# Performance work log

Hardware: AMD Instinct MI355X
Metric: run time of the kernel (lower is better)

Reference implementation:

```python
import jax, jax.numpy as jnp
import numpy as np

B, LQ, LKV, D = 32, 1024, 1024, 512

def setup_inputs() -> dict:
    key = jax.random.key(0)
    kq, kkv = jax.random.split(key)
    query = jax.random.normal(kq, (B, LQ, D), dtype=jnp.float32)
    key_value = jax.random.normal(kkv, (B, LKV, D), dtype=jnp.float32)
    return {"query": query, "key_value": key_value}

def reference(query, key_value):
    # scores: [B, Lq, Lkv] (unscaled dot-product attention)
    scores = jnp.einsum('bqd,bkd->bqk', query, key_value)
    attn_score = jax.nn.softmax(scores, axis=-1)
    # output: [B, Lq, D]
    output = jnp.einsum('bqk,bkd->bqd', attn_score, key_value)
    return (output, attn_score)
```

## Files before the change

### kernel.cpp

```cpp
#include <hip/hip_runtime.h>


constexpr int NB  = 32;
constexpr int LQ  = 1024;
constexpr int LKV = 1024;
constexpr int DD  = 512;

typedef __attribute__((ext_vector_type(4))) float f4;
typedef __attribute__((ext_vector_type(4))) float f32x4;
typedef __attribute__((ext_vector_type(4))) unsigned short u16x4;
typedef __attribute__((ext_vector_type(8))) __bf16 bf16x8;

__device__ __forceinline__ unsigned short f2bf(float x) {
  unsigned u = __builtin_bit_cast(unsigned, x);
  unsigned r = u + 0x7FFFu + ((u >> 16) & 1u);
  return (unsigned short)(r >> 16);
}
__device__ __forceinline__ float bf2f(unsigned short h) {
  unsigned u = ((unsigned)h) << 16;
  return __builtin_bit_cast(float, u);
}

__device__ __forceinline__ void gload16(const void* g, void* l) {
  __builtin_amdgcn_global_load_lds((const __attribute__((address_space(1))) unsigned int*)g,
                                   (__attribute__((address_space(3))) unsigned int*)l,
                                   16, 0, 0);
}

constexpr int PAD = 40;

__global__ __launch_bounds__(256) void gemm_qk_kernel(const float* __restrict__ Q,
                                                      const float* __restrict__ KV,
                                                      float* __restrict__ S)
{
  __shared__ unsigned short Ah[128][PAD], Al[128][PAD], Bh[128][PAD], Bl[128][PAD];
  const int b   = blockIdx.y;
  const int ti  = blockIdx.x >> 3;
  const int tj  = blockIdx.x & 7;
  const int tid  = threadIdx.x;
  const int lane = tid & 63;
  const int wid  = tid >> 6;
  const int wr = (wid >> 1) * 64;
  const int wc = (wid & 1) * 64;

  const float* Qb = Q  + (size_t)b * LQ  * DD + (size_t)ti * 128 * DD;
  const float* Kb = KV + (size_t)b * LKV * DD + (size_t)tj * 128 * DD;

  f32x4 acc[4][4] = {};

  for (int ks = 0; ks < DD; ks += 32) {
    __syncthreads();
#pragma unroll
    for (int i = 0; i < 4; ++i) {
      int idx = tid + i * 256;
      int r   = idx >> 3;
      int k4  = (idx & 7) << 2;
      f4 qa = *(const f4*)(Qb + (size_t)r * DD + ks + k4);
      f4 ka = *(const f4*)(Kb + (size_t)r * DD + ks + k4);
      u16x4 qh, ql, kh, kl;
#pragma unroll
      for (int u = 0; u < 4; ++u) {
        unsigned short h = f2bf(qa[u]);
        qh[u] = h;  ql[u] = f2bf(qa[u] - bf2f(h));
        unsigned short h2 = f2bf(ka[u]);
        kh[u] = h2; kl[u] = f2bf(ka[u] - bf2f(h2));
      }
      *(u16x4*)&Ah[r][k4] = qh;  *(u16x4*)&Al[r][k4] = ql;
      *(u16x4*)&Bh[r][k4] = kh;  *(u16x4*)&Bl[r][k4] = kl;
    }
    __syncthreads();

    const int kf = (lane >> 4) << 3;
    bf16x8 ah[4], al[4], bh[4], bl[4];
#pragma unroll
    for (int m = 0; m < 4; ++m) {
      int row = wr + m * 16 + (lane & 15);
      ah[m] = *(const bf16x8*)&Ah[row][kf];
      al[m] = *(const bf16x8*)&Al[row][kf];
    }
#pragma unroll
    for (int n = 0; n < 4; ++n) {
      int row = wc + n * 16 + (lane & 15);
      bh[n] = *(const bf16x8*)&Bh[row][kf];
      bl[n] = *(const bf16x8*)&Bl[row][kf];
    }
#pragma unroll
    for (int m = 0; m < 4; ++m)
#pragma unroll
      for (int n = 0; n < 4; ++n) {
        acc[m][n] = __builtin_amdgcn_mfma_f32_16x16x32_bf16(ah[m], bh[n], acc[m][n], 0, 0, 0);
        acc[m][n] = __builtin_amdgcn_mfma_f32_16x16x32_bf16(ah[m], bl[n], acc[m][n], 0, 0, 0);
        acc[m][n] = __builtin_amdgcn_mfma_f32_16x16x32_bf16(al[m], bh[n], acc[m][n], 0, 0, 0);
      }
  }

  float* Sb = S + (size_t)b * LQ * LKV;
#pragma unroll
  for (int m = 0; m < 4; ++m) {
    int row0 = ti * 128 + wr + m * 16 + ((lane >> 4) << 2);
#pragma unroll
    for (int n = 0; n < 4; ++n) {
      int col = tj * 128 + wc + n * 16 + (lane & 15);
#pragma unroll
      for (int j = 0; j < 4; ++j)
        Sb[(size_t)(row0 + j) * LKV + col] = acc[m][n][j];
    }
  }
}

__global__ __launch_bounds__(256) void softmax_kernel(float* __restrict__ S)
{
  __shared__ float redmax[4], redsum[4];
  const int tid = threadIdx.x;
  float* p = S + (size_t)blockIdx.x * LKV;

  f4 v = *(const f4*)(p + tid * 4);
  float mx = fmaxf(fmaxf(v[0], v[1]), fmaxf(v[2], v[3]));
#pragma unroll
  for (int off = 32; off >= 1; off >>= 1)
    mx = fmaxf(mx, __shfl_xor(mx, off));
  if ((tid & 63) == 0) redmax[tid >> 6] = mx;
  __syncthreads();
  mx = fmaxf(fmaxf(redmax[0], redmax[1]), fmaxf(redmax[2], redmax[3]));

  f4 e;
#pragma unroll
  for (int u = 0; u < 4; ++u) e[u] = __expf(v[u] - mx);
  float sm = e[0] + e[1] + e[2] + e[3];
#pragma unroll
  for (int off = 32; off >= 1; off >>= 1)
    sm += __shfl_xor(sm, off);
  if ((tid & 63) == 0) redsum[tid >> 6] = sm;
  __syncthreads();
  sm = redsum[0] + redsum[1] + redsum[2] + redsum[3];

  float inv = 1.0f / sm;
  f4 o = { e[0] * inv, e[1] * inv, e[2] * inv, e[3] * inv };
  *(f4*)(p + tid * 4) = o;
}

__global__ __launch_bounds__(256) void kvt_prep_kernel(const float* __restrict__ KV,
                                                       unsigned short* __restrict__ KVT)
{
  __shared__ unsigned short T[64][72];
  const int b  = blockIdx.z;
  const int tk = blockIdx.y;
  const int td = blockIdx.x;
  const int tid = threadIdx.x;

#pragma unroll
  for (int i = 0; i < 4; ++i) {
    int idx = tid + i * 256;
    int r   = idx >> 4;
    int c4  = (idx & 15) << 2;
    f4 v = *(const f4*)(KV + ((size_t)b * LKV + tk * 64 + r) * DD + td * 64 + c4);
    u16x4 h;
#pragma unroll
    for (int u = 0; u < 4; ++u) h[u] = f2bf(v[u]);
    *(u16x4*)&T[r][c4] = h;
  }
  __syncthreads();

#pragma unroll
  for (int i = 0; i < 4; ++i) {
    int idx = tid + i * 256;
    int c   = idx >> 4;
    int r4  = (idx & 15) << 2;
    u16x4 w = { T[r4][c], T[r4 + 1][c], T[r4 + 2][c], T[r4 + 3][c] };
    *(u16x4*)(KVT + ((size_t)b * DD + td * 64 + c) * LKV + tk * 64 + r4) = w;
  }
}

__global__ __launch_bounds__(512) void gemm_av2_kernel(const float* __restrict__ A,
                                                       const unsigned short* __restrict__ KVT,
                                                       float* __restrict__ O)
{
  __shared__ unsigned short Asm[128][72];
  __shared__ unsigned short Bsm[256 * 64];
  const int b  = blockIdx.z;
  const int mi = blockIdx.y;
  const int nj = blockIdx.x;
  const int tid  = threadIdx.x;
  const int lane = tid & 63;
  const int wid  = tid >> 6;
  const int wr = (wid >> 2) * 64;
  const int wc = (wid & 3) * 64;

  const float* Ab = A + (size_t)b * LQ * LKV + (size_t)mi * 128 * LKV;
  const unsigned short* Bb = KVT + ((size_t)b * DD + nj * 256) * LKV;

  f32x4 acc[4][4] = {};

  for (int ks = 0; ks < LKV; ks += 64) {
    __syncthreads();
#pragma unroll
    for (int i = 0; i < 4; ++i) {
      int idx = tid + i * 512;
      int r   = idx >> 4;
      int k4  = (idx & 15) << 2;
      f4 v = *(const f4*)(Ab + (size_t)r * LKV + ks + k4);
      u16x4 h;
#pragma unroll
      for (int u = 0; u < 4; ++u) h[u] = f2bf(v[u]);
      *(u16x4*)&Asm[r][k4] = h;
    }
#pragma unroll
    for (int c = 0; c < 4; ++c) {
      int cc = wid * 4 + c;
      int dd = cc * 8 + (lane >> 3);
      int ss = (lane & 7) ^ (dd & 7);
      const unsigned short* g = Bb + (size_t)dd * LKV + ks + ss * 8;
      gload16(g, &Bsm[cc * 512]);
    }
    __syncthreads();

#pragma unroll
    for (int kk = 0; kk < 64; kk += 32) {
      const int kf = kk + ((lane >> 4) << 3);
      const int cl = kf >> 3;
      bf16x8 af[4], bfv[4];
#pragma unroll
      for (int m = 0; m < 4; ++m)
        af[m] = *(const bf16x8*)&Asm[wr + m * 16 + (lane & 15)][kf];
#pragma unroll
      for (int n = 0; n < 4; ++n) {
        int dd = wc + n * 16 + (lane & 15);
        int sp = cl ^ (dd & 7);
        bfv[n] = *(const bf16x8*)&Bsm[dd * 64 + sp * 8];
      }
#pragma unroll
      for (int m = 0; m < 4; ++m)
#pragma unroll
        for (int n = 0; n < 4; ++n)
          acc[m][n] = __builtin_amdgcn_mfma_f32_16x16x32_bf16(af[m], bfv[n], acc[m][n], 0, 0, 0);
    }
  }

  float* Ob = O + (size_t)b * LQ * DD;
#pragma unroll
  for (int m = 0; m < 4; ++m) {
    int row0 = mi * 128 + wr + m * 16 + ((lane >> 4) << 2);
#pragma unroll
    for (int n = 0; n < 4; ++n) {
      int col = nj * 256 + wc + n * 16 + (lane & 15);
#pragma unroll
      for (int j = 0; j < 4; ++j)
        Ob[(size_t)(row0 + j) * DD + col] = acc[m][n][j];
    }
  }
}

__global__ __launch_bounds__(256) void gemm_av_kernel(const float* __restrict__ A,
                                                      const float* __restrict__ KV,
                                                      float* __restrict__ O)
{
  __shared__ unsigned short Ab[128][PAD], Bt[128][PAD];
  const int b  = blockIdx.z;
  const int mi = blockIdx.y;
  const int nj = blockIdx.x;
  const int tid  = threadIdx.x;
  const int lane = tid & 63;
  const int wid  = tid >> 6;
  const int wr = (wid >> 1) * 64;
  const int wc = (wid & 1) * 64;

  const float* Arow = A  + (size_t)b * LQ * LKV + (size_t)mi * 128 * LKV;
  const float* Kb   = KV + (size_t)b * LKV * DD;

  f32x4 acc[4][4] = {};

  for (int ks = 0; ks < LKV; ks += 32) {
    __syncthreads();
#pragma unroll
    for (int i = 0; i < 4; ++i) {
      int idx = tid + i * 256;
      {
        int r  = idx >> 3;
        int k4 = (idx & 7) << 2;
        f4 av = *(const f4*)(Arow + (size_t)r * LKV + ks + k4);
        u16x4 h;
#pragma unroll
        for (int u = 0; u < 4; ++u) h[u] = f2bf(av[u]);
        *(u16x4*)&Ab[r][k4] = h;
      }
      {
        int kr = idx >> 5;
        int c4 = (idx & 31) << 2;
        f4 kv = *(const f4*)(Kb + (size_t)(ks + kr) * DD + nj * 128 + c4);
        unsigned short hv[4];
#pragma unroll
        for (int u = 0; u < 4; ++u) hv[u] = f2bf(kv[u]);
#pragma unroll
        for (int u = 0; u < 4; ++u) {
          int uu = (u + kr) & 3;
          Bt[c4 + uu][kr] = hv[uu];
        }
      }
    }
    __syncthreads();

    const int kf = (lane >> 4) << 3;
    bf16x8 af[4], bfv[4];
#pragma unroll
    for (int m = 0; m < 4; ++m)
      af[m] = *(const bf16x8*)&Ab[wr + m * 16 + (lane & 15)][kf];
#pragma unroll
    for (int n = 0; n < 4; ++n)
      bfv[n] = *(const bf16x8*)&Bt[wc + n * 16 + (lane & 15)][kf];
#pragma unroll
    for (int m = 0; m < 4; ++m)
#pragma unroll
      for (int n = 0; n < 4; ++n)
        acc[m][n] = __builtin_amdgcn_mfma_f32_16x16x32_bf16(af[m], bfv[n], acc[m][n], 0, 0, 0);
  }

  float* Ob = O + (size_t)b * LQ * DD;
#pragma unroll
  for (int m = 0; m < 4; ++m) {
    int row0 = mi * 128 + wr + m * 16 + ((lane >> 4) << 2);
#pragma unroll
    for (int n = 0; n < 4; ++n) {
      int col = nj * 128 + wc + n * 16 + (lane & 15);
#pragma unroll
      for (int j = 0; j < 4; ++j)
        Ob[(size_t)(row0 + j) * DD + col] = acc[m][n][j];
    }
  }
}

extern "C" void kernel_launch(void* const* d_in, const int* in_sizes, int n_in,
                              void* d_out, int out_size, void* d_ws, size_t ws_size,
                              hipStream_t stream) {
  const float* Q  = (const float*)d_in[0];
  const float* KV = (const float*)d_in[1];
  float* out  = (float*)d_out;
  float* attn = out + (size_t)NB * LQ * DD;

  const size_t kvt_bytes = (size_t)NB * DD * LKV * sizeof(unsigned short);
  const bool use_ws = (ws_size >= kvt_bytes);

  gemm_qk_kernel<<<dim3((LQ / 128) * (LKV / 128), NB), 256, 0, stream>>>(Q, KV, attn);
  if (use_ws) {
    unsigned short* KVT = (unsigned short*)d_ws;
    kvt_prep_kernel<<<dim3(DD / 64, LKV / 64, NB), 256, 0, stream>>>(KV, KVT);
    softmax_kernel<<<dim3(NB * LQ), 256, 0, stream>>>(attn);
    gemm_av2_kernel<<<dim3(DD / 256, LQ / 128, NB), 512, 0, stream>>>(attn, KVT, out);
  } else {
    softmax_kernel<<<dim3(NB * LQ), 256, 0, stream>>>(attn);
    gemm_av_kernel<<<dim3(DD / 128, LQ / 128, NB), 256, 0, stream>>>(attn, KV, out);
  }
}
```

Baseline: 290.7 us.

## Pre-split Q and K into bf16 hi/lo in workspace for QK GEMM

Adds a pass that converts Q to bf16 high/low halves once, and extends the KV prep kernel so it also writes K hi/lo halves. A new QK GEMM then streams these pre-split bf16 tiles into swizzled LDS through global_load_lds, with each wave loading one operand, and runs three bf16 MFMAs per tile pair. The old kernel split fp32 tiles inside every block. The goal is to stop repeating the fp32-to-bf16 split across tiles and to halve the bytes the GEMM loads, at the cost of two extra prep passes and a much larger workspace requirement.

```diff
diff --git a/kernel.cpp b/kernel.cpp
--- a/kernel.cpp
+++ b/kernel.cpp
@@ -28,6 +28,149 @@
 }
 
 constexpr int PAD = 40;
+
+__global__ __launch_bounds__(256) void qsplit_kernel(const float* __restrict__ Q,
+                                                     unsigned short* __restrict__ Qh,
+                                                     unsigned short* __restrict__ Ql)
+{
+  const size_t N = (size_t)NB * LQ * DD;
+  for (size_t i = ((size_t)blockIdx.x * 256 + threadIdx.x) * 4; i < N;
+       i += (size_t)gridDim.x * 256 * 4) {
+    f4 v = *(const f4*)(Q + i);
+    u16x4 h, l;
+#pragma unroll
+    for (int u = 0; u < 4; ++u) {
+      h[u] = f2bf(v[u]);
+      l[u] = f2bf(v[u] - bf2f(h[u]));
+    }
+    *(u16x4*)(Qh + i) = h;
+    *(u16x4*)(Ql + i) = l;
+  }
+}
+
+__global__ __launch_bounds__(256) void kvt_prep2_kernel(const float* __restrict__ KV,
+                                                        unsigned short* __restrict__ Kh,
+                                                        unsigned short* __restrict__ Kl,
+                                                        unsigned short* __restrict__ KVT)
+{
+  __shared__ unsigned short T[64][72];
+  const int b  = blockIdx.z;
+  const int tk = blockIdx.y;
+  const int td = blockIdx.x;
+  const int tid = threadIdx.x;
+
+#pragma unroll
+  for (int i = 0; i < 4; ++i) {
+    int idx = tid + i * 256;
+    int r   = idx >> 4;
+    int c4  = (idx & 15) << 2;
+    size_t goff = ((size_t)b * LKV + tk * 64 + r) * DD + td * 64 + c4;
+    f4 v = *(const f4*)(KV + goff);
+    u16x4 h, l;
+#pragma unroll
+    for (int u = 0; u < 4; ++u) {
+      h[u] = f2bf(v[u]);
+      l[u] = f2bf(v[u] - bf2f(h[u]));
+    }
+    *(u16x4*)&T[r][c4] = h;
+    *(u16x4*)(Kh + goff) = h;
+    *(u16x4*)(Kl + goff) = l;
+  }
+  __syncthreads();
+
+#pragma unroll
+  for (int i = 0; i < 4; ++i) {
+    int idx = tid + i * 256;
+    int c   = idx >> 4;
+    int r4  = (idx & 15) << 2;
+    u16x4 w = { T[r4][c], T[r4 + 1][c], T[r4 + 2][c], T[r4 + 3][c] };
+    *(u16x4*)(KVT + ((size_t)b * DD + td * 64 + c) * LKV + tk * 64 + r4) = w;
+  }
+}
+
+__global__ __launch_bounds__(256) void gemm_qk3_kernel(const unsigned short* __restrict__ Qh,
+                                                       const unsigned short* __restrict__ Ql,
+                                                       const unsigned short* __restrict__ Kh,
+                                                       const unsigned short* __restrict__ Kl,
+                                                       float* __restrict__ S)
+{
+  __shared__ unsigned short SM[4][128 * 64];
+  const int b   = blockIdx.y;
+  const int ti  = blockIdx.x >> 3;
+  const int tj  = blockIdx.x & 7;
+  const int tid  = threadIdx.x;
+  const int lane = tid & 63;
+  const int wid  = tid >> 6;
+  const int wr = (wid >> 1) * 64;
+  const int wc = (wid & 1) * 64;
+
+  const size_t qo = ((size_t)b * LQ  + ti * 128) * DD;
+  const size_t ko = ((size_t)b * LKV + tj * 128) * DD;
+  const unsigned short* tb =
+      (wid == 0) ? Qh + qo : (wid == 1) ? Ql + qo : (wid == 2) ? Kh + ko : Kl + ko;
+
+  const int lrow = lane >> 3;
+  const int ss   = (lane & 7) ^ lrow;
+
+  f32x4 acc[4][4] = {};
+
+  for (int ks = 0; ks < DD; ks += 64) {
+    __syncthreads();
+#pragma unroll
+    for (int i = 0; i < 16; ++i) {
+      const unsigned short* g = tb + (size_t)(i * 8 + lrow) * DD + ks + ss * 8;
+      gload16(g, &SM[wid][i * 512]);
+    }
+    __syncthreads();
+
+#pragma unroll
+    for (int kk = 0; kk < 64; kk += 32) {
+      const int cl  = (kk + ((lane >> 4) << 3)) >> 3;
+      const int sp8 = (cl ^ (lane & 7)) * 8;
+      bf16x8 ah[4], al[4], bh[4], bl[4];
+#pragma unroll
+      for (int m = 0; m < 4; ++m) {
+        int r = wr + m * 16 + (lane & 15);
+        ah[m] = *(const bf16x8*)&SM[0][r * 64 + sp8];
+        al[m] = *(const bf16x8*)&SM[1][r * 64 + sp8];
+      }
+#pragma unroll
+      for (int n = 0; n < 4; ++n) {
+        int r = wc + n * 16 + (lane & 15);
+        bh[n] = *(const bf16x8*)&SM[2][r * 64 + sp8];
+        bl[n] = *(const bf16x8*)&SM[3][r * 64 + sp8];
+      }
+#pragma unroll
+      for (int m = 0; m < 4; ++m)
+#pragma unroll
+        for (int n = 0; n < 4; ++n)
+          acc[m][n] = __builtin_amdgcn_mfma_f32_16x16x32_bf16(ah[m], bh[n], acc[m][n], 0, 0, 0);
+#pragma unroll
+      for (int m = 0; m < 4; ++m)
+#pragma unroll
+        for (int n = 0; n < 4; ++n)
+          acc[m][n] = __builtin_amdgcn_mfma_f32_16x16x32_bf16(ah[m], bl[n], acc[m][n], 0, 0, 0);
+#pragma unroll
+      for (int m = 0; m < 4; ++m)
+#pragma unroll
+        for (int n = 0; n < 4; ++n)
+          acc[m][n] = __builtin_amdgcn_mfma_f32_16x16x32_bf16(al[m], bh[n], acc[m][n], 0, 0, 0);
+    }
+  }
+
+  float* Sb = S + (size_t)b * LQ * LKV;
+#pragma unroll
+  for (int m = 0; m < 4; ++m) {
+    int row0 = ti * 128 + wr + m * 16 + ((lane >> 4) << 2);
+#pragma unroll
+    for (int n = 0; n < 4; ++n) {
+      int col = tj * 128 + wc + n * 16 + (lane & 15);
+#pragma unroll
+      for (int j = 0; j < 4; ++j)
+        Sb[(size_t)(row0 + j) * LKV + col] = acc[m][n][j];
+    }
+  }
+}
 
 __global__ __launch_bounds__(256) void gemm_qk_kernel(const float* __restrict__ Q,
                                                       const float* __restrict__ KV,
@@ -336,16 +479,29 @@
   float* out  = (float*)d_out;
   float* attn = out + (size_t)NB * LQ * DD;
 
-  const size_t kvt_bytes = (size_t)NB * DD * LKV * sizeof(unsigned short);
-  const bool use_ws = (ws_size >= kvt_bytes);
-
-  gemm_qk_kernel<<<dim3((LQ / 128) * (LKV / 128), NB), 256, 0, stream>>>(Q, KV, attn);
-  if (use_ws) {
+  const size_t NQ  = (size_t)NB * LQ * DD;
+  const size_t big_bytes = 5 * NQ * sizeof(unsigned short);
+  const size_t kvt_bytes = NQ * sizeof(unsigned short);
+
+  if (ws_size >= big_bytes) {
+    unsigned short* Qh  = (unsigned short*)d_ws;
+    unsigned short* Qlo = Qh  + NQ;
+    unsigned short* Kh  = Qlo + NQ;
+    unsigned short* Kl  = Kh  + NQ;
+    unsigned short* KVT = Kl  + NQ;
+    qsplit_kernel<<<4096, 256, 0, stream>>>(Q, Qh, Qlo);
+    kvt_prep2_kernel<<<dim3(DD / 64, LKV / 64, NB), 256, 0, stream>>>(KV, Kh, Kl, KVT);
+    gemm_qk3_kernel<<<dim3(64, NB), 256, 0, stream>>>(Qh, Qlo, Kh, Kl, attn);
+    softmax_kernel<<<dim3(NB * LQ), 256, 0, stream>>>(attn);
+    gemm_av2_kernel<<<dim3(DD / 256, LQ / 128, NB), 512, 0, stream>>>(attn, KVT, out);
+  } else if (ws_size >= kvt_bytes) {
     unsigned short* KVT = (unsigned short*)d_ws;
+    gemm_qk_kernel<<<dim3(64, NB), 256, 0, stream>>>(Q, KV, attn);
     kvt_prep_kernel<<<dim3(DD / 64, LKV / 64, NB), 256, 0, stream>>>(KV, KVT);
     softmax_kernel<<<dim3(NB * LQ), 256, 0, stream>>>(attn);
     gemm_av2_kernel<<<dim3(DD / 256, LQ / 128, NB), 512, 0, stream>>>(attn, KVT, out);
   } else {
+    gemm_qk_kernel<<<dim3(64, NB), 256, 0, stream>>>(Q, KV, attn);
     softmax_kernel<<<dim3(NB * LQ), 256, 0, stream>>>(attn);
     gemm_av_kernel<<<dim3(DD / 128, LQ / 128, NB), 256, 0, stream>>>(attn, KV, out);
   }
```

Result: no change. 290.8 us (+0.0%).
